# Optimization experiments

Measured on AMD Instinct MI355X. Metric: run time of the kernel, lower is better.

Reference implementation:

```python
import jax, jax.numpy as jnp
import numpy as np

NC = 3
NA = 3
NO2D = NC + 5
BIN = 2
NO3D = BIN * 3 + 3
STRIDES = (8.0, 16.0, 32.0)
ANCHORS = np.array([[10, 13, 16, 30, 33, 23],
                    [30, 61, 62, 45, 59, 119],
                    [116, 90, 156, 198, 373, 326]], np.float32).reshape(3, NA, 2)
IN_CHES = (256, 512, 1024)
SIZES = ((80, 80), (40, 40), (20, 20))
BS = 8


def _conv(x, w, b, pad):
    y = jax.lax.conv_general_dilated(x, w, (1, 1), ((pad, pad), (pad, pad)),
                                     dimension_numbers=('NCHW', 'OIHW', 'NCHW'))
    return y + b[None, :, None, None]


def setup_inputs() -> dict:
    key = jax.random.key(0)
    d = {}
    k = [0]
    def nk():
        k[0] += 1
        return jax.random.fold_in(key, k[0])
    for i, (c, (ny, nx)) in enumerate(zip(IN_CHES, SIZES)):
        d[f"f{i}"] = jax.random.normal(nk(), (BS, c, ny, nx), jnp.float32)
        d[f"w2a{i}"] = jax.random.normal(nk(), (c, c, 3, 3), jnp.float32) * 0.01
        d[f"b2a{i}"] = jnp.zeros((c,), jnp.float32)
        d[f"w2b{i}"] = jax.random.normal(nk(), (NA * NO2D, c, 1, 1), jnp.float32) * 0.01
        d[f"b2b{i}"] = jnp.zeros((NA * NO2D,), jnp.float32)
        d[f"w3a{i}"] = jax.random.normal(nk(), (c, c, 3, 3), jnp.float32) * 0.01
        d[f"b3a{i}"] = jnp.zeros((c,), jnp.float32)
        d[f"w3b{i}"] = jax.random.normal(nk(), (NA * NO3D, c, 1, 1), jnp.float32) * 0.01
        d[f"b3b{i}"] = jnp.zeros((NA * NO3D,), jnp.float32)
    return d


def _decode(feats, params):
    anchors = jnp.asarray(ANCHORS)  # [L, NA, 2]
    preds = []
    for i in range(3):
        x = feats[i]
        w2a, b2a, w2b, b2b, w3a, b3a, w3b, b3b = params[i]
        # detection heads: 3x3 conv -> 1x1 conv
        h2 = _conv(_conv(x, w2a, b2a, 1), w2b, b2b, 0)  # [bs, na*NO2D, ny, nx]
        h3 = _conv(_conv(x, w3a, b3a, 1), w3b, b3b, 0)  # [bs, na*NO3D, ny, nx]
        bs, _, ny, nx = h2.shape
        h2 = h2.reshape(bs, NA, NO2D, ny, nx).transpose(0, 1, 3, 4, 2)  # [bs,na,ny,nx,NO2D]
        h3 = h3.reshape(bs, NA, NO3D, ny, nx).transpose(0, 1, 3, 4, 2).reshape(bs, -1, NO3D)
        # 2d decode
        p2 = jax.nn.sigmoid(h2)
        yv, xv = jnp.meshgrid(jnp.arange(ny, dtype=jnp.float32),
                              jnp.arange(nx, dtype=jnp.float32), indexing='ij')
        grid = jnp.stack((xv, yv), -1)[None, None]  # [1,1,ny,nx,2]
        xy = (p2[..., 0:2] * 2.0 - 0.5 + grid) * STRIDES[i]
        wh = (p2[..., 2:4] * 2.0) ** 2 * anchors[i][None, :, None, None, :]
        p2 = jnp.concatenate([xy, wh, p2[..., 4:]], -1).reshape(bs, -1, NO2D)
        # 3d decode: bin confidences raw, bin orients L2-normalized, dims sigmoid*2-1
        bins = h3[..., :BIN]
        orient = h3[..., BIN:3 * BIN].reshape(bs, -1, BIN, 2)
        norm = jnp.maximum(jnp.linalg.norm(orient, axis=-1, keepdims=True), 1e-12)
        orient = (orient / norm).reshape(bs, -1, BIN * 2)
        dims = jax.nn.sigmoid(h3[..., -3:]) * 2.0 - 1.0
        p3 = jnp.concatenate([bins, orient, dims], -1)
        preds.append(jnp.concatenate([p2, p3], -1))
    return jnp.concatenate(preds, 1)  # [bs, 25200, NO2D+NO3D]


def reference(f0, f1, f2,
              w2a0, b2a0, w2b0, b2b0, w3a0, b3a0, w3b0, b3b0,
              w2a1, b2a1, w2b1, b2b1, w3a1, b3a1, w3b1, b3b1,
              w2a2, b2a2, w2b2, b2b2, w3a2, b3a2, w3b2, b3b2):
    feats = (f0, f1, f2)
    params = ((w2a0, b2a0, w2b0, b2b0, w3a0, b3a0, w3b0, b3b0),
              (w2a1, b2a1, w2b1, b2b1, w3a1, b3a1, w3b1, b3b1),
              (w2a2, b2a2, w2b2, b2b2, w3a2, b3a2, w3b2, b3b2))
    return _decode(feats, params)
```

## Files before the change

### kernel.cpp

```cpp
#include <hip/hip_runtime.h>
#include <hip/hip_bf16.h>
#include <cstddef>
#include <cstdint>
#include <climits>

#define TOT_ANCH 25200

typedef __bf16 bf16x8 __attribute__((ext_vector_type(8)));
typedef float f32x4 __attribute__((ext_vector_type(4)));

__device__ __forceinline__ float sig_(float x) { return 1.0f / (1.0f + __expf(-x)); }

__device__ __forceinline__ short f2bf(float v) {
  return (short)__builtin_bit_cast(unsigned short, __float2bfloat16(v));
}
__device__ __forceinline__ float bf2f(short v) {
  unsigned int u = ((unsigned int)(unsigned short)v) << 16;
  return __builtin_bit_cast(float, u);
}
__device__ __forceinline__ bf16x8 as_bf16x8(int4 v) { return __builtin_bit_cast(bf16x8, v); }

__device__ __forceinline__ void gload_lds16(const void* g, void* l) {
  __builtin_amdgcn_global_load_lds((const __attribute__((address_space(1))) void*)g,
                                   (__attribute__((address_space(3))) void*)l, 16, 0, 0);
}

__device__ const float d_anch[3][3][2] = {
    {{10.f, 13.f}, {16.f, 30.f}, {33.f, 23.f}},
    {{30.f, 61.f}, {62.f, 45.f}, {59.f, 119.f}},
    {{116.f, 90.f}, {156.f, 198.f}, {373.f, 326.f}}};

struct TrP {
  const float* f; short* fb; int C, HW, ptiles, c32, blk0;
};
struct WtP {
  const float* w; short* dst; long CC, MC, off0; int blk0;
};
struct ConvP {
  const short* fb; const short* wt; const float* bA; const float* bB; short* h;
  int C, H, W, HW, nb_m, nwg, mfast, blk0;
};
struct DeP {
  const short* h; const float* wb; const float* bb;
  int C, Ct, H, W, b0, loff, ptiles, lvl, blk0, nout; float stride;
};

__global__ __launch_bounds__(256) void aux_mega(TrP T0, TrP T1, TrP T2,
                                                WtP J0, WtP J1, WtP J2,
                                                WtP J3, WtP J4, WtP J5, int wt_blk0) {
  __shared__ short tile[32][33];
  int bid = blockIdx.x;
  if (bid >= wt_blk0) {
    WtP J = bid >= J5.blk0 ? J5 : bid >= J4.blk0 ? J4 : bid >= J3.blk0 ? J3 :
            bid >= J2.blk0 ? J2 : bid >= J1.blk0 ? J1 : J0;
    long oi = (long)(bid - J.blk0) * 256 + threadIdx.x;
    if (oi >= J.CC) return;
#pragma unroll
    for (int t = 0; t < 9; ++t) J.dst[t * J.MC + J.off0 + oi] = f2bf(J.w[oi * 9 + t]);
    return;
  }
  TrP T = bid >= T2.blk0 ? T2 : (bid >= T1.blk0 ? T1 : T0);
  int l = bid - T.blk0;
  const int pt = l % T.ptiles; l /= T.ptiles;
  const int cg = l % T.c32;
  const int b = l / T.c32;
  const int p0 = pt * 32, c0 = cg * 32, HW = T.HW, C = T.C;
  const int t = threadIdx.x;
  {
    int cl = t >> 3, pl = (t & 7) * 4;
    int pr = p0 + pl;
    if (pr > HW - 4) pr = HW - 4;
    const float4 v = *(const float4*)(T.f + ((long)b * C + c0 + cl) * HW + pr);
    tile[cl][pl + 0] = f2bf(v.x);
    tile[cl][pl + 1] = f2bf(v.y);
    tile[cl][pl + 2] = f2bf(v.z);
    tile[cl][pl + 3] = f2bf(v.w);
  }
  __syncthreads();
  {
    int pl = t >> 3, cl = (t & 7) * 4;
    int pp = p0 + pl;
    if (pp < HW) {
      int k = pl >> 2;
      int start = p0 + 4 * k;
      if (start > HW - 4) start = HW - 4;
      int col = (start - p0) + (pp - start);
      short4 o;
      o.x = tile[cl + 0][col];
      o.y = tile[cl + 1][col];
      o.z = tile[cl + 2][col];
      o.w = tile[cl + 3][col];
      *(short4*)(T.fb + ((long)b * HW + pp) * C + c0 + cl) = o;
    }
  }
}

__global__ __launch_bounds__(256, 3) void conv3x3_mega(ConvP P0, ConvP P1, ConvP P2,
                                                       const short* zbuf) {
  __shared__ __align__(16) short As[128 * 64];
  __shared__ __align__(16) short Xs[128 * 64];

  int bid = blockIdx.x;
  ConvP P = bid >= P2.blk0 ? P2 : (bid >= P1.blk0 ? P1 : P0);
  const int C = P.C, H = P.H, W = P.W, HW = P.HW, nb_m = P.nb_m, nwg = P.nwg;

  const int orig = bid - P.blk0;
  const int q = nwg >> 3, rr = nwg & 7;
  const int xcd = orig & 7;
  const int wg = (xcd < rr ? xcd * (q + 1) : rr * (q + 1) + (xcd - rr) * q) + (orig >> 3);
  int m, n;
  if (P.mfast) { m = wg % nb_m; n = wg / nb_m; }
  else         { const int nb_n = nwg / nb_m; n = wg % nb_n; m = wg / nb_n; }
  const int mt0 = m * 128;
  const int nt0 = n * 128;
  const int M2 = nb_m * 128;

  const int tid = threadIdx.x;
  const int lane = tid & 63;
  const int wave = tid >> 6;
  const int wm = (wave >> 1) * 64;
  const int wn = (wave & 1) * 64;
  const int s = tid & 7;

  int xs_x[4], xs_y[4];
  int xs_base[4];
  int as_base[4];
#pragma unroll
  for (int r = 0; r < 4; ++r) {
    int cl = r * 32 + (tid >> 3);
    int nn = nt0 + cl;
    int b = nn / HW; int p = nn - b * HW;
    int y = p / W;  int x = p - y * W;
    xs_x[r] = x; xs_y[r] = y;
    int swz = (s ^ (cl & 7)) * 8;
    xs_base[r] = ((b * H + y) * W + x) * C + swz;
    as_base[r] = (mt0 + cl) * C + swz;
  }

  f32x4 acc[4][4];
#pragma unroll
  for (int a_ = 0; a_ < 4; ++a_)
#pragma unroll
    for (int b_ = 0; b_ < 4; ++b_) acc[a_][b_] = (f32x4){0.f, 0.f, 0.f, 0.f};

  const int nkb = C >> 6;
  const long MC = (long)M2 * C;
  const short* gzb = zbuf + s * 8;

  for (int kb = 0; kb < nkb; ++kb) {
    const int kb64 = kb << 6;
    for (int t = 0; t < 9; ++t) {
      const int dy = t / 3 - 1, dx = t - (t / 3) * 3 - 1;
      const int doff = (dy * W + dx) * C + kb64;
      const short* gap = P.wt + (long)t * MC + kb64;
#pragma unroll
      for (int r = 0; r < 4; ++r) {
        gload_lds16(gap + as_base[r], (char*)As + r * 4096 + tid * 16);
        bool ok = ((unsigned)(xs_y[r] + dy) < (unsigned)H) &
                  ((unsigned)(xs_x[r] + dx) < (unsigned)W);
        const short* gx = ok ? P.fb + xs_base[r] + doff : gzb;
        gload_lds16(gx, (char*)Xs + r * 4096 + tid * 16);
      }
      __syncthreads();

#pragma unroll
      for (int ks = 0; ks < 2; ++ks) {
        bf16x8 af[4], xf[4];
#pragma unroll
        for (int mf = 0; mf < 4; ++mf) {
          int row = wm + mf * 16 + (lane & 15);
          int c = (ks * 4 + (lane >> 4)) ^ (row & 7);
          af[mf] = as_bf16x8(*(const int4*)((const char*)As + row * 128 + c * 16));
        }
#pragma unroll
        for (int nf = 0; nf < 4; ++nf) {
          int col = wn + nf * 16 + (lane & 15);
          int c = (ks * 4 + (lane >> 4)) ^ (col & 7);
          xf[nf] = as_bf16x8(*(const int4*)((const char*)Xs + col * 128 + c * 16));
        }
        __builtin_amdgcn_s_setprio(1);
#pragma unroll
        for (int mf = 0; mf < 4; ++mf)
#pragma unroll
          for (int nf = 0; nf < 4; ++nf)
            acc[mf][nf] = __builtin_amdgcn_mfma_f32_16x16x32_bf16(af[mf], xf[nf],
                                                                  acc[mf][nf], 0, 0, 0);
        __builtin_amdgcn_s_setprio(0);
      }
      __syncthreads();
    }
  }

  int nb[4], np[4];
#pragma unroll
  for (int nf = 0; nf < 4; ++nf) {
    int nn = nt0 + wn + nf * 16 + (lane & 15);
    nb[nf] = nn / HW;
    np[nf] = nn - nb[nf] * HW;
  }
#pragma unroll
  for (int mf = 0; mf < 4; ++mf) {
    int co0 = mt0 + wm + mf * 16 + (lane >> 4) * 4;
#pragma unroll
    for (int rg = 0; rg < 4; ++rg) {
      int co = co0 + rg;
      float bv = co < C ? P.bA[co] : P.bB[co - C];
#pragma unroll
      for (int nf = 0; nf < 4; ++nf) {
        float v = acc[mf][nf][rg] + bv;
        P.h[((long)nb[nf] * M2 + co) * HW + np[nf]] = f2bf(v);
      }
    }
  }
}

__global__ __launch_bounds__(256) void decode_mega2(DeP D0, DeP D1, DeP D2,
                                                    DeP D3, DeP D4, DeP D5,
                                                    float* __restrict__ out) {
  __shared__ float htile[32][33];
  __shared__ float wtileT[32][32];
  __shared__ float otile[32][28];
  int bid = blockIdx.x;
  DeP D = bid >= D5.blk0 ? D5 : bid >= D4.blk0 ? D4 : bid >= D3.blk0 ? D3 :
          bid >= D2.blk0 ? D2 : bid >= D1.blk0 ? D1 : D0;
  int l = bid - D.blk0;
  const int pt = l % D.ptiles;
  const int bl = l / D.ptiles;
  const int C = D.C, Ct = D.Ct, H = D.H, W = D.W, HW = H * W;
  const int nout = D.nout;
  const int t = threadIdx.x;
  const int p0 = pt * 32;
  const int px = t & 31, og = t >> 5;

  float acc[4] = {0.f, 0.f, 0.f, 0.f};
  const int nch = C >> 5;
  for (int ch = 0; ch < nch; ++ch) {
    const int c0 = ch << 5;
    {
      int cl = t >> 3, pl = (t & 7) * 4;
      int pr = p0 + pl;
      if (pr > HW - 4) pr = HW - 4;
      const short4 v = *(const short4*)(D.h + ((long)bl * Ct + c0 + cl) * HW + pr);
      htile[cl][pl + 0] = bf2f(v.x);
      htile[cl][pl + 1] = bf2f(v.y);
      htile[cl][pl + 2] = bf2f(v.z);
      htile[cl][pl + 3] = bf2f(v.w);
    }
    {
      int j = t >> 3, cl = (t & 7) * 4;
      if (j < nout) {
        const float4 v = *(const float4*)(D.wb + (long)j * C + c0 + cl);
        wtileT[cl + 0][j] = v.x;
        wtileT[cl + 1][j] = v.y;
        wtileT[cl + 2][j] = v.z;
        wtileT[cl + 3][j] = v.w;
      } else {
        wtileT[cl + 0][j] = 0.f;
        wtileT[cl + 1][j] = 0.f;
        wtileT[cl + 2][j] = 0.f;
        wtileT[cl + 3][j] = 0.f;
      }
    }
    __syncthreads();
#pragma unroll
    for (int c = 0; c < 32; ++c) {
      float v = htile[c][px];
      const float4 wv = *(const float4*)&wtileT[c][og * 4];
      acc[0] = fmaf(v, wv.x, acc[0]);
      acc[1] = fmaf(v, wv.y, acc[1]);
      acc[2] = fmaf(v, wv.z, acc[2]);
      acc[3] = fmaf(v, wv.w, acc[3]);
    }
    __syncthreads();
  }
#pragma unroll
  for (int g = 0; g < 4; ++g) {
    int j = og * 4 + g;
    if (j < nout) otile[px][j] = acc[g] + D.bb[j];
  }
  __syncthreads();

  if (t < 96) {
    const int pxx = t / 3, a = t - (t / 3) * 3;
    const int p = p0 + pxx;
    if (p < HW) {
      float* o = out + ((size_t)(D.b0 + bl) * TOT_ANCH + D.loff + (size_t)a * HW + p) * 17;
      if (nout == 24) {
        const int y = p / W, x = p - (p / W) * W;
        float s0 = sig_(otile[pxx][a * 8 + 0]);
        float s1 = sig_(otile[pxx][a * 8 + 1]);
        float sw = sig_(otile[pxx][a * 8 + 2]) * 2.f;
        float sh = sig_(otile[pxx][a * 8 + 3]) * 2.f;
        o[0] = (s0 * 2.f - 0.5f + (float)x) * D.stride;
        o[1] = (s1 * 2.f - 0.5f + (float)y) * D.stride;
        o[2] = sw * sw * d_anch[D.lvl][a][0];
        o[3] = sh * sh * d_anch[D.lvl][a][1];
        o[4] = sig_(otile[pxx][a * 8 + 4]);
        o[5] = sig_(otile[pxx][a * 8 + 5]);
        o[6] = sig_(otile[pxx][a * 8 + 6]);
        o[7] = sig_(otile[pxx][a * 8 + 7]);
      } else {
        float v0 = otile[pxx][a * 9 + 0], v1 = otile[pxx][a * 9 + 1];
        float v2 = otile[pxx][a * 9 + 2], v3 = otile[pxx][a * 9 + 3];
        float v4 = otile[pxx][a * 9 + 4], v5 = otile[pxx][a * 9 + 5];
        float v6 = otile[pxx][a * 9 + 6], v7 = otile[pxx][a * 9 + 7];
        float v8 = otile[pxx][a * 9 + 8];
        float n0 = fmaxf(sqrtf(v2 * v2 + v3 * v3), 1e-12f);
        float n1 = fmaxf(sqrtf(v4 * v4 + v5 * v5), 1e-12f);
        o[8] = v0;
        o[9] = v1;
        o[10] = v2 / n0;
        o[11] = v3 / n0;
        o[12] = v4 / n1;
        o[13] = v5 / n1;
        o[14] = sig_(v6) * 2.f - 1.f;
        o[15] = sig_(v7) * 2.f - 1.f;
        o[16] = sig_(v8) * 2.f - 1.f;
      }
    }
  }
}


static inline size_t al256(size_t x) { return (x + 255) & ~(size_t)255; }

extern "C" void kernel_launch(void* const* d_in, const int* in_sizes, int n_in,
                              void* d_out, int out_size, void* d_ws, size_t ws_size,
                              hipStream_t stream) {
  (void)in_sizes; (void)n_in; (void)out_size;
  char* ws = (char*)d_ws;
  float* out = (float*)d_out;

  hipMemsetAsync(ws, 0, 256, stream);
  const short* zb = (const short*)ws;

  struct Lvl { int C, H, W, loff; float stride; };
  const Lvl L[3] = {{256, 80, 80, 0, 8.f}, {512, 40, 40, 19200, 16.f},
                    {1024, 20, 20, 24000, 32.f}};
  const int B = 8;
  const int ord[3] = {2, 1, 0};

  const float* f_[3]; const float *w2a_[3], *b2a_[3], *w2b_[3], *b2b_[3];
  const float *w3a_[3], *b3a_[3], *w3b_[3], *b3b_[3];
  int HW_[3], ptiles_[3], c32_[3], nbm_[3], mfast_[3];
  long CC_[3];
  size_t fbB_[3], wtB_[3], hB_[3];
  for (int i = 0; i < 3; ++i) {
    f_[i]   = (const float*)d_in[9 * i + 0];
    w2a_[i] = (const float*)d_in[9 * i + 1];
    b2a_[i] = (const float*)d_in[9 * i + 2];
    w2b_[i] = (const float*)d_in[9 * i + 3];
    b2b_[i] = (const float*)d_in[9 * i + 4];
    w3a_[i] = (const float*)d_in[9 * i + 5];
    b3a_[i] = (const float*)d_in[9 * i + 6];
    w3b_[i] = (const float*)d_in[9 * i + 7];
    b3b_[i] = (const float*)d_in[9 * i + 8];
    const int C = L[i].C;
    HW_[i] = L[i].H * L[i].W;
    ptiles_[i] = (HW_[i] + 31) / 32;
    c32_[i] = C / 32;
    nbm_[i] = (2 * C) / 128;
    CC_[i] = (long)C * C;
    fbB_[i] = (size_t)B * HW_[i] * C * 2;
    wtB_[i] = (size_t)36 * CC_[i];
    hB_[i]  = (size_t)B * HW_[i] * 2 * C * 2;
    mfast_[i] = ((size_t)B * HW_[i] * C >= (size_t)18 * CC_[i]) ? 1 : 0;
  }

  size_t off = 256;
  size_t fb_o[3], wt_o[3], h_o[3];
  for (int i = 0; i < 3; ++i) { fb_o[i] = off; off += al256(fbB_[i]); }
  for (int i = 0; i < 3; ++i) { wt_o[i] = off; off += al256(wtB_[i]); }
  for (int i = 0; i < 3; ++i) { h_o[i] = off; off += al256(hB_[i]); }

  if (off <= ws_size) {
    short* fb[3]; short* wtb[3]; short* hb[3];
    for (int i = 0; i < 3; ++i) {
      fb[i] = (short*)(ws + fb_o[i]);
      wtb[i] = (short*)(ws + wt_o[i]);
      hb[i] = (short*)(ws + h_o[i]);
    }
    TrP T[3]; int tb = 0;
    for (int i = 0; i < 3; ++i) {
      T[i] = TrP{f_[i], fb[i], L[i].C, HW_[i], ptiles_[i], c32_[i], tb};
      tb += ptiles_[i] * c32_[i] * B;
    }
    WtP J[6]; int jb = tb;
    for (int i = 0; i < 3; ++i) {
      J[2 * i]     = WtP{w2a_[i], wtb[i], CC_[i], 2 * CC_[i], 0, jb};
      jb += (int)(CC_[i] / 256);
      J[2 * i + 1] = WtP{w3a_[i], wtb[i], CC_[i], 2 * CC_[i], CC_[i], jb};
      jb += (int)(CC_[i] / 256);
    }
    aux_mega<<<jb, 256, 0, stream>>>(T[0], T[1], T[2], J[0], J[1], J[2], J[3], J[4],
                                     J[5], tb);

    ConvP P[3]; int cb = 0;
    for (int k = 0; k < 3; ++k) {
      const int i = ord[k];
      int nwg = (B * HW_[i] / 128) * nbm_[i];
      P[k] = ConvP{fb[i], wtb[i], b2a_[i], b3a_[i], hb[i],
                   L[i].C, L[i].H, L[i].W, HW_[i], nbm_[i], nwg, mfast_[i], cb};
      cb += nwg;
    }
    conv3x3_mega<<<cb, 256, 0, stream>>>(P[0], P[1], P[2], zb);

    DeP D[6]; int db = 0;
    for (int k = 0; k < 3; ++k) {
      const int i = ord[k];
      const int C = L[i].C;
      D[2 * k] = DeP{hb[i], w2b_[i], b2b_[i], C, 2 * C, L[i].H, L[i].W,
                     0, L[i].loff, ptiles_[i], i, db, 24, L[i].stride};
      db += ptiles_[i] * B;
      D[2 * k + 1] = DeP{hb[i] + (size_t)C * HW_[i], w3b_[i], b3b_[i], C, 2 * C,
                         L[i].H, L[i].W, 0, L[i].loff, ptiles_[i], i, db, 27,
                         L[i].stride};
      db += ptiles_[i] * B;
    }
    decode_mega2<<<db, 256, 0, stream>>>(D[0], D[1], D[2], D[3], D[4], D[5], out);
    return;
  }

  for (int i = 0; i < 3; ++i) {
    const int C = L[i].C, HW = HW_[i];
    int Bg = B;
    for (int cand = 1; cand <= 8; cand <<= 1) {
      int bg = B / cand;
      if (((long)bg * HW) % 128) continue;
      size_t need = 256 + al256((size_t)bg * HW * C * 2) + al256(wtB_[i]) +
                    (size_t)bg * HW * 2 * C * 2;
      if (need <= ws_size) { Bg = bg; break; }
    }
    size_t fo = 256;
    size_t wo = fo + al256((size_t)Bg * HW * C * 2);
    size_t ho = wo + al256(wtB_[i]);
    short* fb = (short*)(ws + fo);
    short* wtb = (short*)(ws + wo);
    short* hb = (short*)(ws + ho);

    TrP TZ{};
    WtP J0 = WtP{w2a_[i], wtb, CC_[i], 2 * CC_[i], 0, 0};
    WtP J1 = WtP{w3a_[i], wtb, CC_[i], 2 * CC_[i], CC_[i], (int)(CC_[i] / 256)};
    WtP JX = J1; JX.blk0 = INT_MAX;
    aux_mega<<<(int)(2 * CC_[i] / 256), 256, 0, stream>>>(TZ, TZ, TZ, J0, J1, JX, JX,
                                                          JX, JX, 0);

    const int nbg = B / Bg;
    for (int g = 0; g < nbg; ++g) {
      const int b0 = g * Bg;
      TrP T0 = TrP{f_[i] + (size_t)b0 * C * HW, fb, C, HW, ptiles_[i], c32_[i], 0};
      TrP TX = T0; TX.blk0 = INT_MAX;
      WtP JZ{}; JZ.blk0 = INT_MAX;
      aux_mega<<<ptiles_[i] * c32_[i] * Bg, 256, 0, stream>>>(T0, TX, TX, JZ, JZ, JZ,
                                                              JZ, JZ, JZ, INT_MAX);

      int nwg = (Bg * HW / 128) * nbm_[i];
      ConvP P0 = ConvP{fb, wtb, b2a_[i], b3a_[i], hb, C, L[i].H, L[i].W, HW,
                       nbm_[i], nwg, mfast_[i], 0};
      ConvP PX = P0; PX.blk0 = INT_MAX;
      conv3x3_mega<<<nwg, 256, 0, stream>>>(P0, PX, PX, zb);

      DeP D0 = DeP{hb, w2b_[i], b2b_[i], C, 2 * C, L[i].H, L[i].W,
                   b0, L[i].loff, ptiles_[i], i, 0, 24, L[i].stride};
      DeP D1 = DeP{hb + (size_t)C * HW, w3b_[i], b3b_[i], C, 2 * C, L[i].H, L[i].W,
                   b0, L[i].loff, ptiles_[i], i, ptiles_[i] * Bg, 27, L[i].stride};
      DeP DX = D1; DX.blk0 = INT_MAX;
      decode_mega2<<<2 * ptiles_[i] * Bg, 256, 0, stream>>>(D0, D1, DX, DX, DX, DX,
                                                            out);
    }
  }
}
```

Measured before the change: 486.9 us.

## Enlarge conv3x3 GEMM tile to 256x256 with 8 waves and double-buffered LDS

The implicit-GEMM conv kernel moves from 128x128 tiles with 4 waves to 256x256 tiles with 8 waves (512 threads). LDS staging becomes a double buffer, so global-to-LDS loads for the next K-step are issued while MFMAs run on the current buffer. The aim is more data reuse per loaded byte and hiding global load latency. A bounds mask on N handles partial tiles, and the XCD remapping is simplified. In exchange, LDS use (128 KB) and register pressure rise sharply, occupancy drops to one block per CU, and the grid shrinks, which may leave CUs idle on the small level.

```diff
diff --git a/kernel.cpp b/kernel.cpp
--- a/kernel.cpp
+++ b/kernel.cpp
@@ -38,7 +38,7 @@
 };
 struct ConvP {
   const short* fb; const short* wt; const float* bA; const float* bB; short* h;
-  int C, H, W, HW, nb_m, nwg, mfast, blk0;
+  int C, H, W, HW, Ng, nb_m, nwg, mfast, blk0;
 };
 struct DeP {
   const short* h; const float* wb; const float* bb;
@@ -95,120 +95,174 @@
   }
 }
 
-__global__ __launch_bounds__(256, 3) void conv3x3_mega(ConvP P0, ConvP P1, ConvP P2,
-                                                       const short* zbuf) {
-  __shared__ __align__(16) short As[128 * 64];
-  __shared__ __align__(16) short Xs[128 * 64];
+__global__ __launch_bounds__(512) void conv3x3_mega(ConvP P0, ConvP P1, ConvP P2,
+                                                    const short* zbuf) {
+  __shared__ __align__(16) short As[2][2][128 * 64];
+  __shared__ __align__(16) short Xs[2][2][128 * 64];
 
   int bid = blockIdx.x;
   ConvP P = bid >= P2.blk0 ? P2 : (bid >= P1.blk0 ? P1 : P0);
-  const int C = P.C, H = P.H, W = P.W, HW = P.HW, nb_m = P.nb_m, nwg = P.nwg;
+  const int C = P.C, H = P.H, W = P.W, HW = P.HW, Ng = P.Ng;
+  const int nb_m = P.nb_m, nwg = P.nwg;
 
   const int orig = bid - P.blk0;
-  const int q = nwg >> 3, rr = nwg & 7;
-  const int xcd = orig & 7;
-  const int wg = (xcd < rr ? xcd * (q + 1) : rr * (q + 1) + (xcd - rr) * q) + (orig >> 3);
+  int wg;
+  if (nwg & 7) {
+    wg = orig;
+  } else {
+    const int q = nwg >> 3;
+    const int xcd = orig & 7;
+    wg = xcd * q + (orig >> 3);
+  }
   int m, n;
   if (P.mfast) { m = wg % nb_m; n = wg / nb_m; }
   else         { const int nb_n = nwg / nb_m; n = wg % nb_n; m = wg / nb_n; }
-  const int mt0 = m * 128;
-  const int nt0 = n * 128;
-  const int M2 = nb_m * 128;
+  const int mt0 = m * 256;
+  const int nt0 = n * 256;
+  const int M2 = nb_m * 256;
 
   const int tid = threadIdx.x;
   const int lane = tid & 63;
   const int wave = tid >> 6;
-  const int wm = (wave >> 1) * 64;
-  const int wn = (wave & 1) * 64;
-  const int s = tid & 7;
-
-  int xs_x[4], xs_y[4];
-  int xs_base[4];
-  int as_base[4];
-#pragma unroll
-  for (int r = 0; r < 4; ++r) {
-    int cl = r * 32 + (tid >> 3);
+  const int wm = wave >> 2;
+  const int wn = wave & 3;
+  const int xh = wn >> 1;
+  const int xc0 = (wn & 1) * 64;
+
+  const int sr = tid >> 3;
+  const int swz = ((tid & 7) ^ (sr & 7)) * 8;
+  int xs_x[4], xs_y[4], xs_base[4], xs_ok[4], as_base[4];
+#pragma unroll
+  for (int hr = 0; hr < 4; ++hr) {
+    int cl = (hr >> 1) * 128 + (hr & 1) * 64 + sr;
     int nn = nt0 + cl;
-    int b = nn / HW; int p = nn - b * HW;
-    int y = p / W;  int x = p - y * W;
-    xs_x[r] = x; xs_y[r] = y;
-    int swz = (s ^ (cl & 7)) * 8;
-    xs_base[r] = ((b * H + y) * W + x) * C + swz;
-    as_base[r] = (mt0 + cl) * C + swz;
-  }
-
-  f32x4 acc[4][4];
-#pragma unroll
-  for (int a_ = 0; a_ < 4; ++a_)
+    int ok = nn < Ng;
+    int nnc = ok ? nn : 0;
+    int b = nnc / HW; int p = nnc - b * HW;
+    int y = p / W;    int x = p - y * W;
+    xs_x[hr] = x; xs_y[hr] = y; xs_ok[hr] = ok;
+    xs_base[hr] = ((b * H + y) * W + x) * C + swz;
+    as_base[hr] = (mt0 + cl) * C + swz;
+  }
+
+  f32x4 acc[8][4];
+#pragma unroll
+  for (int a_ = 0; a_ < 8; ++a_)
 #pragma unroll
     for (int b_ = 0; b_ < 4; ++b_) acc[a_][b_] = (f32x4){0.f, 0.f, 0.f, 0.f};
 
   const int nkb = C >> 6;
+  const int nkt = nkb * 9;
   const long MC = (long)M2 * C;
-  const short* gzb = zbuf + s * 8;
-
-  for (int kb = 0; kb < nkb; ++kb) {
-    const int kb64 = kb << 6;
-    for (int t = 0; t < 9; ++t) {
-      const int dy = t / 3 - 1, dx = t - (t / 3) * 3 - 1;
-      const int doff = (dy * W + dx) * C + kb64;
-      const short* gap = P.wt + (long)t * MC + kb64;
-#pragma unroll
-      for (int r = 0; r < 4; ++r) {
-        gload_lds16(gap + as_base[r], (char*)As + r * 4096 + tid * 16);
-        bool ok = ((unsigned)(xs_y[r] + dy) < (unsigned)H) &
-                  ((unsigned)(xs_x[r] + dx) < (unsigned)W);
-        const short* gx = ok ? P.fb + xs_base[r] + doff : gzb;
-        gload_lds16(gx, (char*)Xs + r * 4096 + tid * 16);
-      }
-      __syncthreads();
-
-#pragma unroll
-      for (int ks = 0; ks < 2; ++ks) {
-        bf16x8 af[4], xf[4];
-#pragma unroll
-        for (int mf = 0; mf < 4; ++mf) {
-          int row = wm + mf * 16 + (lane & 15);
-          int c = (ks * 4 + (lane >> 4)) ^ (row & 7);
-          af[mf] = as_bf16x8(*(const int4*)((const char*)As + row * 128 + c * 16));
+  const short* gzb = zbuf + swz;
+
+  auto stageA = [&](int bu, int h, const short* gap) {
+#pragma unroll
+    for (int r = 0; r < 2; ++r)
+      gload_lds16(gap + as_base[h * 2 + r],
+                  (char*)&As[bu][h][0] + r * 8192 + tid * 16);
+  };
+  auto stageX = [&](int bu, int h, int dy, int dx, int doff) {
+#pragma unroll
+    for (int r = 0; r < 2; ++r) {
+      int hr = h * 2 + r;
+      bool ok = xs_ok[hr] & ((unsigned)(xs_y[hr] + dy) < (unsigned)H) &
+                ((unsigned)(xs_x[hr] + dx) < (unsigned)W);
+      const short* gx = ok ? P.fb + xs_base[hr] + doff : gzb;
+      gload_lds16(gx, (char*)&Xs[bu][h][0] + r * 8192 + tid * 16);
+    }
+  };
+
+  {
+    const short* gap = P.wt;
+    stageA(0, 0, gap);
+    stageA(0, 1, gap);
+    stageX(0, 0, -1, -1, (-1 * W - 1) * C);
+    stageX(0, 1, -1, -1, (-1 * W - 1) * C);
+    asm volatile("s_waitcnt vmcnt(0)" ::: "memory");
+    __builtin_amdgcn_sched_barrier(0);
+    __builtin_amdgcn_s_barrier();
+  }
+
+  int ntt = 1, nkb64 = 0;
+  for (int kt = 0; kt < nkt; ++kt) {
+    const int cur = kt & 1;
+    const int nxt = cur ^ 1;
+    const bool hasn = (kt + 1) < nkt;
+    const int tdiv3n = ntt / 3;
+    const int dyn = tdiv3n - 1, dxn = ntt - tdiv3n * 3 - 1;
+    const int doffn = (dyn * W + dxn) * C + nkb64;
+    const short* gapn = P.wt + (long)ntt * MC + nkb64;
+
+    const char* Ah = (const char*)&As[cur][wm][0];
+    const char* Xh = (const char*)&Xs[cur][xh][0];
+
+    bf16x8 xf[4];
+#pragma unroll
+    for (int ph = 0; ph < 4; ++ph) {
+      const int ks = ph >> 1, mh = ph & 1;
+      if (mh == 0) {
+#pragma unroll
+        for (int nf = 0; nf < 4; ++nf) {
+          int cl = xc0 + nf * 16 + (lane & 15);
+          int c = (ks * 4 + (lane >> 4)) ^ (cl & 7);
+          xf[nf] = as_bf16x8(*(const int4*)(Xh + cl * 128 + c * 16));
         }
-#pragma unroll
-        for (int nf = 0; nf < 4; ++nf) {
-          int col = wn + nf * 16 + (lane & 15);
-          int c = (ks * 4 + (lane >> 4)) ^ (col & 7);
-          xf[nf] = as_bf16x8(*(const int4*)((const char*)Xs + col * 128 + c * 16));
-        }
-        __builtin_amdgcn_s_setprio(1);
-#pragma unroll
-        for (int mf = 0; mf < 4; ++mf)
-#pragma unroll
-          for (int nf = 0; nf < 4; ++nf)
-            acc[mf][nf] = __builtin_amdgcn_mfma_f32_16x16x32_bf16(af[mf], xf[nf],
-                                                                  acc[mf][nf], 0, 0, 0);
-        __builtin_amdgcn_s_setprio(0);
-      }
-      __syncthreads();
-    }
-  }
-
-  int nb[4], np[4];
+      }
+      bf16x8 af[4];
+#pragma unroll
+      for (int mf = 0; mf < 4; ++mf) {
+        int rl = mh * 64 + mf * 16 + (lane & 15);
+        int c = (ks * 4 + (lane >> 4)) ^ (rl & 7);
+        af[mf] = as_bf16x8(*(const int4*)(Ah + rl * 128 + c * 16));
+      }
+      if (hasn) {
+        if (ph == 0) stageA(nxt, 0, gapn);
+        else if (ph == 1) stageA(nxt, 1, gapn);
+        else if (ph == 2) { stageX(nxt, 0, dyn, dxn, doffn); stageX(nxt, 1, dyn, dxn, doffn); }
+      }
+      __builtin_amdgcn_s_barrier();
+      asm volatile("s_waitcnt lgkmcnt(0)" ::: "memory");
+      __builtin_amdgcn_sched_barrier(0);
+      __builtin_amdgcn_s_setprio(1);
+#pragma unroll
+      for (int mf = 0; mf < 4; ++mf)
+#pragma unroll
+        for (int nf = 0; nf < 4; ++nf)
+          acc[mh * 4 + mf][nf] = __builtin_amdgcn_mfma_f32_16x16x32_bf16(
+              af[mf], xf[nf], acc[mh * 4 + mf][nf], 0, 0, 0);
+      __builtin_amdgcn_s_setprio(0);
+      if (ph == 3) {
+        asm volatile("s_waitcnt vmcnt(0)" ::: "memory");
+        __builtin_amdgcn_sched_barrier(0);
+      }
+      __builtin_amdgcn_s_barrier();
+    }
+    if (++ntt == 9) { ntt = 0; nkb64 += 64; }
+  }
+
+  int nbv[4], npv[4], nok[4];
 #pragma unroll
   for (int nf = 0; nf < 4; ++nf) {
-    int nn = nt0 + wn + nf * 16 + (lane & 15);
-    nb[nf] = nn / HW;
-    np[nf] = nn - nb[nf] * HW;
-  }
-#pragma unroll
-  for (int mf = 0; mf < 4; ++mf) {
-    int co0 = mt0 + wm + mf * 16 + (lane >> 4) * 4;
+    int nn = nt0 + wn * 64 + nf * 16 + (lane & 15);
+    nok[nf] = nn < Ng;
+    int nnc = nok[nf] ? nn : 0;
+    nbv[nf] = nnc / HW;
+    npv[nf] = nnc - nbv[nf] * HW;
+  }
+#pragma unroll
+  for (int mfg = 0; mfg < 8; ++mfg) {
+    int co0 = mt0 + wm * 128 + mfg * 16 + (lane >> 4) * 4;
 #pragma unroll
     for (int rg = 0; rg < 4; ++rg) {
       int co = co0 + rg;
       float bv = co < C ? P.bA[co] : P.bB[co - C];
 #pragma unroll
       for (int nf = 0; nf < 4; ++nf) {
-        float v = acc[mf][nf][rg] + bv;
-        P.h[((long)nb[nf] * M2 + co) * HW + np[nf]] = f2bf(v);
+        if (nok[nf]) {
+          float v = acc[mfg][nf][rg] + bv;
+          P.h[((long)nbv[nf] * M2 + co) * HW + npv[nf]] = f2bf(v);
+        }
       }
     }
   }
@@ -359,7 +413,7 @@
     HW_[i] = L[i].H * L[i].W;
     ptiles_[i] = (HW_[i] + 31) / 32;
     c32_[i] = C / 32;
-    nbm_[i] = (2 * C) / 128;
+    nbm_[i] = (2 * C) / 256;
     CC_[i] = (long)C * C;
     fbB_[i] = (size_t)B * HW_[i] * C * 2;
     wtB_[i] = (size_t)36 * CC_[i];
@@ -398,12 +452,14 @@
     ConvP P[3]; int cb = 0;
     for (int k = 0; k < 3; ++k) {
       const int i = ord[k];
-      int nwg = (B * HW_[i] / 128) * nbm_[i];
+      const int Ng = B * HW_[i];
+      const int ntn = (Ng + 255) / 256;
+      const int nwg = ntn * nbm_[i];
       P[k] = ConvP{fb[i], wtb[i], b2a_[i], b3a_[i], hb[i],
-                   L[i].C, L[i].H, L[i].W, HW_[i], nbm_[i], nwg, mfast_[i], cb};
+                   L[i].C, L[i].H, L[i].W, HW_[i], Ng, nbm_[i], nwg, mfast_[i], cb};
       cb += nwg;
     }
-    conv3x3_mega<<<cb, 256, 0, stream>>>(P[0], P[1], P[2], zb);
+    conv3x3_mega<<<cb, 512, 0, stream>>>(P[0], P[1], P[2], zb);
 
     DeP D[6]; int db = 0;
     for (int k = 0; k < 3; ++k) {
@@ -426,7 +482,6 @@
     int Bg = B;
     for (int cand = 1; cand <= 8; cand <<= 1) {
       int bg = B / cand;
-      if (((long)bg * HW) % 128) continue;
       size_t need = 256 + al256((size_t)bg * HW * C * 2) + al256(wtB_[i]) +
                     (size_t)bg * HW * 2 * C * 2;
       if (need <= ws_size) { Bg = bg; break; }
@@ -454,11 +509,13 @@
       aux_mega<<<ptiles_[i] * c32_[i] * Bg, 256, 0, stream>>>(T0, TX, TX, JZ, JZ, JZ,
                                                               JZ, JZ, JZ, INT_MAX);
 
-      int nwg = (Bg * HW / 128) * nbm_[i];
-      ConvP P0 = ConvP{fb, wtb, b2a_[i], b3a_[i], hb, C, L[i].H, L[i].W, HW,
-                       nbm_[i], nwg, mfast_[i], 0};
-      ConvP PX = P0; PX.blk0 = INT_MAX;
-      conv3x3_mega<<<nwg, 256, 0, stream>>>(P0, PX, PX, zb);
+      const int Ng = Bg * HW;
+      const int ntn = (Ng + 255) / 256;
+      const int nwg = ntn * nbm_[i];
+      ConvP Pc = ConvP{fb, wtb, b2a_[i], b3a_[i], hb, C, L[i].H, L[i].W, HW,
+                       Ng, nbm_[i], nwg, mfast_[i], 0};
+      ConvP PX = Pc; PX.blk0 = INT_MAX;
+      conv3x3_mega<<<nwg, 512, 0, stream>>>(Pc, PX, PX, zb);
 
       DeP D0 = DeP{hb, w2b_[i], b2b_[i], C, 2 * C, L[i].H, L[i].W,
                    b0, L[i].loff, ptiles_[i], i, 0, 24, L[i].stride};
```

Result: slower. 556.9 us (+14.4%).

## Merge 1x1 decode heads into one MFMA GEMM over pixel-major conv output

Applied to the files above, without the earlier changes.

The conv3x3 epilogue now writes its output pixel-major (channels contiguous) with packed short4 stores instead of channel-major scattered bf16 stores. A new prep kernel builds a combined zero-padded bf16 weight matrix for both 1x1 heads, and the decode kernel computes both heads at once using bf16 MFMA instead of scalar fp32 FMAs, with bias added in the epilogue. This removes the second decode pass over the intermediate tensor and the slow scalar inner loop. It adds a small weight-prep launch and rounds the 1x1 weights to bf16.

```diff
diff --git a/kernel.cpp b/kernel.cpp
--- a/kernel.cpp
+++ b/kernel.cpp
@@ -36,13 +36,16 @@
 struct WtP {
   const float* w; short* dst; long CC, MC, off0; int blk0;
 };
+struct WcP {
+  const float* w2b; const float* w3b; short* wc; int csh2, blk0;
+};
 struct ConvP {
   const short* fb; const short* wt; const float* bA; const float* bB; short* h;
   int C, H, W, HW, nb_m, nwg, mfast, blk0;
 };
 struct DeP {
-  const short* h; const float* wb; const float* bb;
-  int C, Ct, H, W, b0, loff, ptiles, lvl, blk0, nout; float stride;
+  const short* h; const short* wc; const float* bb2; const float* bb3;
+  int C2, H, W, b0, loff, ptiles, lvl, blk0; float stride;
 };
 
 __global__ __launch_bounds__(256) void aux_mega(TrP T0, TrP T1, TrP T2,
@@ -95,6 +98,24 @@
   }
 }
 
+__global__ __launch_bounds__(256) void wc_prep(WcP K0, WcP K1, WcP K2) {
+  int bid = blockIdx.x;
+  WcP K = bid >= K2.blk0 ? K2 : (bid >= K1.blk0 ? K1 : K0);
+  int idx = (bid - K.blk0) * 256 + threadIdx.x;
+  const int C2 = 1 << K.csh2;
+  if (idx >= 64 * C2) return;
+  const int row = idx >> K.csh2;
+  const int c = idx & (C2 - 1);
+  const int C = C2 >> 1;
+  float v = 0.f;
+  if (row < 24) {
+    if (c < C) v = K.w2b[row * C + c];
+  } else if (row < 51) {
+    if (c >= C) v = K.w3b[(row - 24) * C + (c - C)];
+  }
+  K.wc[idx] = f2bf(v);
+}
+
 __global__ __launch_bounds__(256, 3) void conv3x3_mega(ConvP P0, ConvP P1, ConvP P2,
                                                        const short* zbuf) {
   __shared__ __align__(16) short As[128 * 64];
@@ -191,92 +212,98 @@
     }
   }
 
-  int nb[4], np[4];
+  long nbase[4];
 #pragma unroll
   for (int nf = 0; nf < 4; ++nf) {
     int nn = nt0 + wn + nf * 16 + (lane & 15);
-    nb[nf] = nn / HW;
-    np[nf] = nn - nb[nf] * HW;
+    int nb = nn / HW;
+    int np = nn - nb * HW;
+    nbase[nf] = ((long)nb * HW + np) * M2;
   }
 #pragma unroll
   for (int mf = 0; mf < 4; ++mf) {
     int co0 = mt0 + wm + mf * 16 + (lane >> 4) * 4;
+    float bv[4];
 #pragma unroll
     for (int rg = 0; rg < 4; ++rg) {
       int co = co0 + rg;
-      float bv = co < C ? P.bA[co] : P.bB[co - C];
-#pragma unroll
-      for (int nf = 0; nf < 4; ++nf) {
-        float v = acc[mf][nf][rg] + bv;
-        P.h[((long)nb[nf] * M2 + co) * HW + np[nf]] = f2bf(v);
-      }
-    }
-  }
-}
-
-__global__ __launch_bounds__(256) void decode_mega2(DeP D0, DeP D1, DeP D2,
-                                                    DeP D3, DeP D4, DeP D5,
-                                                    float* __restrict__ out) {
-  __shared__ float htile[32][33];
-  __shared__ float wtileT[32][32];
-  __shared__ float otile[32][28];
+      bv[rg] = co < C ? P.bA[co] : P.bB[co - C];
+    }
+#pragma unroll
+    for (int nf = 0; nf < 4; ++nf) {
+      short4 o;
+      o.x = f2bf(acc[mf][nf][0] + bv[0]);
+      o.y = f2bf(acc[mf][nf][1] + bv[1]);
+      o.z = f2bf(acc[mf][nf][2] + bv[2]);
+      o.w = f2bf(acc[mf][nf][3] + bv[3]);
+      *(short4*)(P.h + nbase[nf] + co0) = o;
+    }
+  }
+}
+
+__global__ __launch_bounds__(256) void decode_v3(DeP D0, DeP D1, DeP D2,
+                                                 float* __restrict__ out) {
+  __shared__ __align__(16) short htileT[32][136];
+  __shared__ __align__(16) short Wtile[64][136];
+  __shared__ float otile[32][52];
   int bid = blockIdx.x;
-  DeP D = bid >= D5.blk0 ? D5 : bid >= D4.blk0 ? D4 : bid >= D3.blk0 ? D3 :
-          bid >= D2.blk0 ? D2 : bid >= D1.blk0 ? D1 : D0;
+  DeP D = bid >= D2.blk0 ? D2 : (bid >= D1.blk0 ? D1 : D0);
   int l = bid - D.blk0;
   const int pt = l % D.ptiles;
   const int bl = l / D.ptiles;
-  const int C = D.C, Ct = D.Ct, H = D.H, W = D.W, HW = H * W;
-  const int nout = D.nout;
+  const int C2 = D.C2, H = D.H, W = D.W, HW = H * W;
   const int t = threadIdx.x;
+  const int lane = t & 63;
+  const int wv = t >> 6;
   const int p0 = pt * 32;
-  const int px = t & 31, og = t >> 5;
-
-  float acc[4] = {0.f, 0.f, 0.f, 0.f};
-  const int nch = C >> 5;
-  for (int ch = 0; ch < nch; ++ch) {
-    const int c0 = ch << 5;
-    {
-      int cl = t >> 3, pl = (t & 7) * 4;
-      int pr = p0 + pl;
-      if (pr > HW - 4) pr = HW - 4;
-      const short4 v = *(const short4*)(D.h + ((long)bl * Ct + c0 + cl) * HW + pr);
-      htile[cl][pl + 0] = bf2f(v.x);
-      htile[cl][pl + 1] = bf2f(v.y);
-      htile[cl][pl + 2] = bf2f(v.z);
-      htile[cl][pl + 3] = bf2f(v.w);
-    }
-    {
-      int j = t >> 3, cl = (t & 7) * 4;
-      if (j < nout) {
-        const float4 v = *(const float4*)(D.wb + (long)j * C + c0 + cl);
-        wtileT[cl + 0][j] = v.x;
-        wtileT[cl + 1][j] = v.y;
-        wtileT[cl + 2][j] = v.z;
-        wtileT[cl + 3][j] = v.w;
-      } else {
-        wtileT[cl + 0][j] = 0.f;
-        wtileT[cl + 1][j] = 0.f;
-        wtileT[cl + 2][j] = 0.f;
-        wtileT[cl + 3][j] = 0.f;
+
+  const short* hB = D.h + (long)bl * HW * C2;
+
+  f32x4 acc[2];
+  acc[0] = (f32x4){0.f, 0.f, 0.f, 0.f};
+  acc[1] = (f32x4){0.f, 0.f, 0.f, 0.f};
+
+  const int rounds = C2 >> 7;
+  for (int rd = 0; rd < rounds; ++rd) {
+    const int c0 = rd << 7;
+#pragma unroll
+    for (int r = 0; r < 2; ++r) {
+      int idx = r * 256 + t;
+      int px = idx >> 4, kc = idx & 15;
+      int p = p0 + px;
+      int pc = p < HW ? p : HW - 1;
+      int4 v = *(const int4*)(hB + (long)pc * C2 + c0 + kc * 8);
+      *(int4*)&htileT[px][kc * 8] = v;
+    }
+#pragma unroll
+    for (int r = 0; r < 4; ++r) {
+      int idx = r * 256 + t;
+      int row = idx >> 4, kc = idx & 15;
+      int4 v = *(const int4*)(D.wc + (long)row * C2 + c0 + kc * 8);
+      *(int4*)&Wtile[row][kc * 8] = v;
+    }
+    __syncthreads();
+#pragma unroll
+    for (int st = 0; st < 4; ++st) {
+      const int k0 = st * 32 + (lane >> 4) * 8;
+      bf16x8 af = as_bf16x8(*(const int4*)&Wtile[wv * 16 + (lane & 15)][k0]);
+#pragma unroll
+      for (int nf = 0; nf < 2; ++nf) {
+        bf16x8 xf = as_bf16x8(*(const int4*)&htileT[nf * 16 + (lane & 15)][k0]);
+        acc[nf] = __builtin_amdgcn_mfma_f32_16x16x32_bf16(af, xf, acc[nf], 0, 0, 0);
       }
     }
     __syncthreads();
-#pragma unroll
-    for (int c = 0; c < 32; ++c) {
-      float v = htile[c][px];
-      const float4 wv = *(const float4*)&wtileT[c][og * 4];
-      acc[0] = fmaf(v, wv.x, acc[0]);
-      acc[1] = fmaf(v, wv.y, acc[1]);
-      acc[2] = fmaf(v, wv.z, acc[2]);
-      acc[3] = fmaf(v, wv.w, acc[3]);
-    }
-    __syncthreads();
-  }
-#pragma unroll
-  for (int g = 0; g < 4; ++g) {
-    int j = og * 4 + g;
-    if (j < nout) otile[px][j] = acc[g] + D.bb[j];
+  }
+
+#pragma unroll
+  for (int nf = 0; nf < 2; ++nf) {
+    int px = nf * 16 + (lane & 15);
+#pragma unroll
+    for (int rg = 0; rg < 4; ++rg) {
+      int row = wv * 16 + (lane >> 4) * 4 + rg;
+      if (row < 51) otile[px][row] = acc[nf][rg];
+    }
   }
   __syncthreads();
 
@@ -285,26 +312,35 @@
     const int p = p0 + pxx;
     if (p < HW) {
       float* o = out + ((size_t)(D.b0 + bl) * TOT_ANCH + D.loff + (size_t)a * HW + p) * 17;
-      if (nout == 24) {
+      {
         const int y = p / W, x = p - (p / W) * W;
-        float s0 = sig_(otile[pxx][a * 8 + 0]);
-        float s1 = sig_(otile[pxx][a * 8 + 1]);
-        float sw = sig_(otile[pxx][a * 8 + 2]) * 2.f;
-        float sh = sig_(otile[pxx][a * 8 + 3]) * 2.f;
+        float h0 = otile[pxx][a * 8 + 0] + D.bb2[a * 8 + 0];
+        float h1 = otile[pxx][a * 8 + 1] + D.bb2[a * 8 + 1];
+        float h2 = otile[pxx][a * 8 + 2] + D.bb2[a * 8 + 2];
+        float h3 = otile[pxx][a * 8 + 3] + D.bb2[a * 8 + 3];
+        float s0 = sig_(h0);
+        float s1 = sig_(h1);
+        float sw = sig_(h2) * 2.f;
+        float sh = sig_(h3) * 2.f;
         o[0] = (s0 * 2.f - 0.5f + (float)x) * D.stride;
         o[1] = (s1 * 2.f - 0.5f + (float)y) * D.stride;
         o[2] = sw * sw * d_anch[D.lvl][a][0];
         o[3] = sh * sh * d_anch[D.lvl][a][1];
-        o[4] = sig_(otile[pxx][a * 8 + 4]);
-        o[5] = sig_(otile[pxx][a * 8 + 5]);
-        o[6] = sig_(otile[pxx][a * 8 + 6]);
-        o[7] = sig_(otile[pxx][a * 8 + 7]);
-      } else {
-        float v0 = otile[pxx][a * 9 + 0], v1 = otile[pxx][a * 9 + 1];
-        float v2 = otile[pxx][a * 9 + 2], v3 = otile[pxx][a * 9 + 3];
-        float v4 = otile[pxx][a * 9 + 4], v5 = otile[pxx][a * 9 + 5];
-        float v6 = otile[pxx][a * 9 + 6], v7 = otile[pxx][a * 9 + 7];
-        float v8 = otile[pxx][a * 9 + 8];
+        o[4] = sig_(otile[pxx][a * 8 + 4] + D.bb2[a * 8 + 4]);
+        o[5] = sig_(otile[pxx][a * 8 + 5] + D.bb2[a * 8 + 5]);
+        o[6] = sig_(otile[pxx][a * 8 + 6] + D.bb2[a * 8 + 6]);
+        o[7] = sig_(otile[pxx][a * 8 + 7] + D.bb2[a * 8 + 7]);
+      }
+      {
+        float v0 = otile[pxx][24 + a * 9 + 0] + D.bb3[a * 9 + 0];
+        float v1 = otile[pxx][24 + a * 9 + 1] + D.bb3[a * 9 + 1];
+        float v2 = otile[pxx][24 + a * 9 + 2] + D.bb3[a * 9 + 2];
+        float v3 = otile[pxx][24 + a * 9 + 3] + D.bb3[a * 9 + 3];
+        float v4 = otile[pxx][24 + a * 9 + 4] + D.bb3[a * 9 + 4];
+        float v5 = otile[pxx][24 + a * 9 + 5] + D.bb3[a * 9 + 5];
+        float v6 = otile[pxx][24 + a * 9 + 6] + D.bb3[a * 9 + 6];
+        float v7 = otile[pxx][24 + a * 9 + 7] + D.bb3[a * 9 + 7];
+        float v8 = otile[pxx][24 + a * 9 + 8] + D.bb3[a * 9 + 8];
         float n0 = fmaxf(sqrtf(v2 * v2 + v3 * v3), 1e-12f);
         float n1 = fmaxf(sqrtf(v4 * v4 + v5 * v5), 1e-12f);
         o[8] = v0;
@@ -342,9 +378,9 @@
 
   const float* f_[3]; const float *w2a_[3], *b2a_[3], *w2b_[3], *b2b_[3];
   const float *w3a_[3], *b3a_[3], *w3b_[3], *b3b_[3];
-  int HW_[3], ptiles_[3], c32_[3], nbm_[3], mfast_[3];
+  int HW_[3], ptiles_[3], c32_[3], nbm_[3], mfast_[3], csh2_[3];
   long CC_[3];
-  size_t fbB_[3], wtB_[3], hB_[3];
+  size_t fbB_[3], wtB_[3], hB_[3], wcB_[3];
   for (int i = 0; i < 3; ++i) {
     f_[i]   = (const float*)d_in[9 * i + 0];
     w2a_[i] = (const float*)d_in[9 * i + 1];
@@ -361,24 +397,28 @@
     c32_[i] = C / 32;
     nbm_[i] = (2 * C) / 128;
     CC_[i] = (long)C * C;
+    csh2_[i] = (C == 256) ? 9 : (C == 512) ? 10 : 11;
     fbB_[i] = (size_t)B * HW_[i] * C * 2;
     wtB_[i] = (size_t)36 * CC_[i];
     hB_[i]  = (size_t)B * HW_[i] * 2 * C * 2;
+    wcB_[i] = (size_t)64 * 2 * C * 2;
     mfast_[i] = ((size_t)B * HW_[i] * C >= (size_t)18 * CC_[i]) ? 1 : 0;
   }
 
   size_t off = 256;
-  size_t fb_o[3], wt_o[3], h_o[3];
+  size_t fb_o[3], wt_o[3], h_o[3], wc_o[3];
   for (int i = 0; i < 3; ++i) { fb_o[i] = off; off += al256(fbB_[i]); }
   for (int i = 0; i < 3; ++i) { wt_o[i] = off; off += al256(wtB_[i]); }
+  for (int i = 0; i < 3; ++i) { wc_o[i] = off; off += al256(wcB_[i]); }
   for (int i = 0; i < 3; ++i) { h_o[i] = off; off += al256(hB_[i]); }
 
   if (off <= ws_size) {
-    short* fb[3]; short* wtb[3]; short* hb[3];
+    short* fb[3]; short* wtb[3]; short* hb[3]; short* wcb[3];
     for (int i = 0; i < 3; ++i) {
       fb[i] = (short*)(ws + fb_o[i]);
       wtb[i] = (short*)(ws + wt_o[i]);
       hb[i] = (short*)(ws + h_o[i]);
+      wcb[i] = (short*)(ws + wc_o[i]);
     }
     TrP T[3]; int tb = 0;
     for (int i = 0; i < 3; ++i) {
@@ -394,6 +434,12 @@
     }
     aux_mega<<<jb, 256, 0, stream>>>(T[0], T[1], T[2], J[0], J[1], J[2], J[3], J[4],
                                      J[5], tb);
+    WcP K[3]; int kb = 0;
+    for (int i = 0; i < 3; ++i) {
+      K[i] = WcP{w2b_[i], w3b_[i], wcb[i], csh2_[i], kb};
+      kb += (64 * 2 * L[i].C) / 256;
+    }
+    wc_prep<<<kb, 256, 0, stream>>>(K[0], K[1], K[2]);
 
     ConvP P[3]; int cb = 0;
     for (int k = 0; k < 3; ++k) {
@@ -405,19 +451,14 @@
     }
     conv3x3_mega<<<cb, 256, 0, stream>>>(P[0], P[1], P[2], zb);
 
-    DeP D[6]; int db = 0;
+    DeP D[3]; int db = 0;
     for (int k = 0; k < 3; ++k) {
       const int i = ord[k];
-      const int C = L[i].C;
-      D[2 * k] = DeP{hb[i], w2b_[i], b2b_[i], C, 2 * C, L[i].H, L[i].W,
-                     0, L[i].loff, ptiles_[i], i, db, 24, L[i].stride};
+      D[k] = DeP{hb[i], wcb[i], b2b_[i], b3b_[i], 2 * L[i].C, L[i].H, L[i].W,
+                 0, L[i].loff, ptiles_[i], i, db, L[i].stride};
       db += ptiles_[i] * B;
-      D[2 * k + 1] = DeP{hb[i] + (size_t)C * HW_[i], w3b_[i], b3b_[i], C, 2 * C,
-                         L[i].H, L[i].W, 0, L[i].loff, ptiles_[i], i, db, 27,
-                         L[i].stride};
-      db += ptiles_[i] * B;
-    }
-    decode_mega2<<<db, 256, 0, stream>>>(D[0], D[1], D[2], D[3], D[4], D[5], out);
+    }
+    decode_v3<<<db, 256, 0, stream>>>(D[0], D[1], D[2], out);
     return;
   }
 
@@ -428,14 +469,16 @@
       int bg = B / cand;
       if (((long)bg * HW) % 128) continue;
       size_t need = 256 + al256((size_t)bg * HW * C * 2) + al256(wtB_[i]) +
-                    (size_t)bg * HW * 2 * C * 2;
+                    al256(wcB_[i]) + (size_t)bg * HW * 2 * C * 2;
       if (need <= ws_size) { Bg = bg; break; }
     }
     size_t fo = 256;
     size_t wo = fo + al256((size_t)Bg * HW * C * 2);
-    size_t ho = wo + al256(wtB_[i]);
+    size_t co = wo + al256(wtB_[i]);
+    size_t ho = co + al256(wcB_[i]);
     short* fb = (short*)(ws + fo);
     short* wtb = (short*)(ws + wo);
+    short* wcb = (short*)(ws + co);
     short* hb = (short*)(ws + ho);
 
     TrP TZ{};
@@ -444,6 +487,9 @@
     WtP JX = J1; JX.blk0 = INT_MAX;
     aux_mega<<<(int)(2 * CC_[i] / 256), 256, 0, stream>>>(TZ, TZ, TZ, J0, J1, JX, JX,
                                                           JX, JX, 0);
+    WcP K0 = WcP{w2b_[i], w3b_[i], wcb, csh2_[i], 0};
+    WcP KX = K0; KX.blk0 = INT_MAX;
+    wc_prep<<<(64 * 2 * C) / 256, 256, 0, stream>>>(K0, KX, KX);
 
     const int nbg = B / Bg;
     for (int g = 0; g < nbg; ++g) {
@@ -455,18 +501,15 @@
                                                               JZ, JZ, JZ, INT_MAX);
 
       int nwg = (Bg * HW / 128) * nbm_[i];
-      ConvP P0 = ConvP{fb, wtb, b2a_[i], b3a_[i], hb, C, L[i].H, L[i].W, HW,
+      ConvP Pc = ConvP{fb, wtb, b2a_[i], b3a_[i], hb, C, L[i].H, L[i].W, HW,
                        nbm_[i], nwg, mfast_[i], 0};
-      ConvP PX = P0; PX.blk0 = INT_MAX;
-      conv3x3_mega<<<nwg, 256, 0, stream>>>(P0, PX, PX, zb);
-
-      DeP D0 = DeP{hb, w2b_[i], b2b_[i], C, 2 * C, L[i].H, L[i].W,
-                   b0, L[i].loff, ptiles_[i], i, 0, 24, L[i].stride};
-      DeP D1 = DeP{hb + (size_t)C * HW, w3b_[i], b3b_[i], C, 2 * C, L[i].H, L[i].W,
-                   b0, L[i].loff, ptiles_[i], i, ptiles_[i] * Bg, 27, L[i].stride};
-      DeP DX = D1; DX.blk0 = INT_MAX;
-      decode_mega2<<<2 * ptiles_[i] * Bg, 256, 0, stream>>>(D0, D1, DX, DX, DX, DX,
-                                                            out);
-    }
-  }
-}
+      ConvP PX = Pc; PX.blk0 = INT_MAX;
+      conv3x3_mega<<<nwg, 256, 0, stream>>>(Pc, PX, PX, zb);
+
+      DeP D0 = DeP{hb, wcb, b2b_[i], b3b_[i], 2 * C, L[i].H, L[i].W,
+                   b0, L[i].loff, ptiles_[i], i, 0, L[i].stride};
+      DeP DX = D0; DX.blk0 = INT_MAX;
+      decode_v3<<<ptiles_[i] * Bg, 256, 0, stream>>>(D0, DX, DX, out);
+    }
+  }
+}
```

Measured after the change: 423.0 us, median of 2. 13.1% less time.
